# Kernel tuning notes

Hardware: AMD Instinct MI355X
Metric: run time of the kernel (lower is better)

The kernel has to match this reference:

```python
import jax, jax.numpy as jnp
import numpy as np

TEMPERATURE = 1.0
EXAGGERATION = 1.0


def setup_inputs() -> dict:
    key = jax.random.key(0)
    features = jax.random.normal(key, (8192, 128), dtype=jnp.float32)
    return {"features": features}


def _cauchy_sim(x, y):
    # 1 / ((cdist(x,y) * t)^2 + 1) == 1 / (t^2 * sq_dist + 1)
    sq = (
        jnp.sum(x * x, axis=1)[:, None]
        + jnp.sum(y * y, axis=1)[None, :]
        - 2.0 * (x @ y.T)
    )
    sq = jnp.maximum(sq, 0.0)  # numerical floor, matches cdist >= 0
    return 1.0 / (sq * (TEMPERATURE * TEMPERATURE) + 1.0)


def reference(features):
    batch_size = features.shape[0] // 2
    a = features[:batch_size]
    b = features[batch_size:]

    sim_aa = _cauchy_sim(a, a)  # [B, B]
    sim_bb = _cauchy_sim(b, b)  # [B, B]
    sim_ab = _cauchy_sim(a, b)  # [B, B]

    tempered_alignment = jnp.mean(jnp.log(jnp.diagonal(sim_ab)))

    self_mask = jnp.eye(batch_size, dtype=bool)
    sim_aa = jnp.where(self_mask, 0.0, sim_aa)
    sim_bb = jnp.where(self_mask, 0.0, sim_bb)

    # hstack((sim_ab.T, sim_bb)).sum(1) == sim_ab.sum(0) + sim_bb.sum(1)
    logsumexp_1 = jnp.mean(jnp.log(jnp.sum(sim_ab, axis=0) + jnp.sum(sim_bb, axis=1)))
    logsumexp_2 = jnp.mean(jnp.log(jnp.sum(sim_aa, axis=1) + jnp.sum(sim_ab, axis=1)))
    raw_uniformity = logsumexp_1 + logsumexp_2

    loss = -(EXAGGERATION * tempered_alignment - raw_uniformity / 2.0)
    return loss
```

## Files before the change

kernel.cpp:

```cpp
#include <hip/hip_runtime.h>
#include <hip/hip_bf16.h>
#include <hip/hip_fp8.h>

typedef float f32x4 __attribute__((ext_vector_type(4)));
typedef int   i32x4 __attribute__((ext_vector_type(4)));
typedef int   i32x8 __attribute__((ext_vector_type(8)));

static constexpr int D     = 128;
static constexpr int BATCH = 4096;
static constexpr int N     = 8192;
static constexpr int BT    = 128;
static constexpr int NT    = N / BT;
static constexpr int TRI   = NT * (NT + 1) / 2;
static constexpr int SCALE1 = 0x7F7F7F7F;

__device__ __forceinline__ void load_lds16(const void* g, void* l) {
    __builtin_amdgcn_global_load_lds(
        (const __attribute__((address_space(1))) unsigned int*)g,
        (__attribute__((address_space(3))) unsigned int*)l, 16, 0, 0);
}

__global__ __launch_bounds__(256) void prep_kernel(const float* __restrict__ f,
                                                   unsigned char* __restrict__ Fp8,
                                                   float* __restrict__ norms,
                                                   float* __restrict__ diag,
                                                   float* __restrict__ out) {
    if (blockIdx.x == 0 && threadIdx.x == 0) out[0] = 0.f;
    const int w = threadIdx.x >> 6, lane = threadIdx.x & 63;
    const int i = blockIdx.x * 4 + w;
    const float2 va = *(const float2*)(f + (size_t)i * D + lane * 2);
    const float2 vb = *(const float2*)(f + (size_t)(i + BATCH) * D + lane * 2);

    auto storeF = [&](int row, float x, float y) {
        union { unsigned char b[2]; unsigned short u; } pk;
        pk.b[0] = __hip_fp8_e4m3(x).__x;
        pk.b[1] = __hip_fp8_e4m3(y).__x;
        const size_t dst = (size_t)(row >> 7) * 16384 + (row & 127) * 128
                         + (((lane >> 3) ^ (row & 7)) << 4) + (lane & 7) * 2;
        *(unsigned short*)(Fp8 + dst) = pk.u;
    };
    storeF(i, va.x, va.y);
    storeF(i + BATCH, vb.x, vb.y);

    float na = va.x * va.x + va.y * va.y;
    float nb = vb.x * vb.x + vb.y * vb.y;
    const float dx = va.x - vb.x, dy = va.y - vb.y;
    float dd = dx * dx + dy * dy;
    #pragma unroll
    for (int m = 1; m <= 32; m <<= 1) {
        na += __shfl_xor(na, m); nb += __shfl_xor(nb, m); dd += __shfl_xor(dd, m);
    }
    if (lane == 0) {
        norms[i] = na; norms[i + BATCH] = nb;
        diag[i] = 1.f / (dd + 1.f);
    }
}

__global__ __launch_bounds__(256, 4) void tile_kernel(const unsigned char* __restrict__ Fp8,
                                                      const float* __restrict__ norms,
                                                      float* __restrict__ P) {
    const int bid = blockIdx.x;
    const int id = (bid & 7) * (TRI / 8) + (bid >> 3);
    int ti = (int)((sqrtf(8.f * (float)id + 1.f) - 1.f) * 0.5f);
    while ((ti + 1) * (ti + 2) / 2 <= id) ++ti;
    while (ti * (ti + 1) / 2 > id) --ti;
    const int tj = id - ti * (ti + 1) / 2;
    const bool diagblk = (ti == tj);

    __shared__ __align__(16) unsigned char As[16384];
    __shared__ __align__(16) unsigned char Bs[16384];
    __shared__ float colbuf[BT];

    const int tid = threadIdx.x, wv = tid >> 6, lane = tid & 63;
    const int lr = lane & 15, hk = lane >> 4;
    if (tid < BT) colbuf[tid] = 0.f;

    const unsigned char* Aimg = Fp8 + (size_t)ti * 16384;
    const unsigned char* Bimg = Fp8 + (size_t)tj * 16384;
    #pragma unroll
    for (int it = 0; it < 4; ++it)
        load_lds16(Aimg + (it * 256 + tid) * 16, As + it * 4096 + wv * 1024);
    #pragma unroll
    for (int it = 0; it < 4; ++it)
        load_lds16(Bimg + (it * 256 + tid) * 16, Bs + it * 4096 + wv * 1024);
    __syncthreads();

    auto frag = [&](const unsigned char* S, int rowbase) -> i32x8 {
        const int row = rowbase + lr;
        const i32x4 q0 = *(const i32x4*)(S + row * 128 + (((hk * 2 + 0) ^ (lr & 7)) << 4));
        const i32x4 q1 = *(const i32x4*)(S + row * 128 + (((hk * 2 + 1) ^ (lr & 7)) << 4));
        return __builtin_shufflevector(q0, q1, 0, 1, 2, 3, 4, 5, 6, 7);
    };

    f32x4 acc[2][8];
    #pragma unroll
    for (int i = 0; i < 2; ++i)
        #pragma unroll
        for (int j = 0; j < 8; ++j)
            acc[i][j] = (f32x4){0.f, 0.f, 0.f, 0.f};

    const i32x8 av0 = frag(As, wv * 32);
    const i32x8 av1 = frag(As, wv * 32 + 16);
    #pragma unroll
    for (int fj = 0; fj < 8; ++fj) {
        const i32x8 bv = frag(Bs, fj * 16);
        acc[0][fj] = __builtin_amdgcn_mfma_scale_f32_16x16x128_f8f6f4(
            av0, bv, acc[0][fj], 0, 0, 0, SCALE1, 0, SCALE1);
        acc[1][fj] = __builtin_amdgcn_mfma_scale_f32_16x16x128_f8f6f4(
            av1, bv, acc[1][fj], 0, 0, 0, SCALE1, 0, SCALE1);
    }

    float colN[8];
    #pragma unroll
    for (int fj = 0; fj < 8; ++fj)
        colN[fj] = norms[tj * BT + fj * 16 + lr];

    float* PR = P + ((size_t)ti * NT + tj) * BT;
    #pragma unroll
    for (int fi = 0; fi < 2; ++fi) {
        const int lrow = wv * 32 + fi * 16 + hk * 4;
        const f32x4 rN = *(const f32x4*)(norms + ti * BT + lrow);
        f32x4 rs = (f32x4){0.f, 0.f, 0.f, 0.f};
        #pragma unroll
        for (int fj = 0; fj < 8; ++fj) {
            const int lcol = fj * 16 + lr;
            #pragma unroll
            for (int r = 0; r < 4; ++r) {
                float sq = rN[r] + colN[fj] - 2.f * acc[fi][fj][r];
                sq = fmaxf(sq, 0.f);
                float sim = __builtin_amdgcn_rcpf(sq + 1.f);
                if (diagblk && (lrow + r == lcol)) sim = 0.f;
                rs[r] += sim;
                acc[fi][fj][r] = sim;
            }
        }
        #pragma unroll
        for (int r = 0; r < 4; ++r) {
            rs[r] += __shfl_xor(rs[r], 1);
            rs[r] += __shfl_xor(rs[r], 2);
            rs[r] += __shfl_xor(rs[r], 4);
            rs[r] += __shfl_xor(rs[r], 8);
        }
        if (lr == 0)
            *(f32x4*)(PR + lrow) = rs;
    }

    if (!diagblk) {
        #pragma unroll
        for (int fj = 0; fj < 8; ++fj) {
            float cs = 0.f;
            #pragma unroll
            for (int fi = 0; fi < 2; ++fi)
                #pragma unroll
                for (int r = 0; r < 4; ++r)
                    cs += acc[fi][fj][r];
            cs += __shfl_xor(cs, 16);
            cs += __shfl_xor(cs, 32);
            if (hk == 0)
                atomicAdd(&colbuf[fj * 16 + lr], cs);
        }
        __syncthreads();
        if (tid < BT)
            P[((size_t)tj * NT + ti) * BT + tid] = colbuf[tid];
    }
}

__global__ __launch_bounds__(128) void finalize_kernel(const float* __restrict__ P,
                                                       const float* __restrict__ diag,
                                                       float* __restrict__ out) {
    const int t = blockIdx.x;
    const int r = threadIdx.x;
    const float* base = P + (size_t)t * NT * BT + r;
    float s = 0.f;
    #pragma unroll 8
    for (int k = 0; k < NT; ++k) s += base[k * BT];
    const int i = t * BT + r;
    float term = 0.5f * __logf(s);
    if (i >= BATCH) term -= __logf(diag[i - BATCH]);
    #pragma unroll
    for (int m = 1; m <= 32; m <<= 1) term += __shfl_xor(term, m);
    if ((threadIdx.x & 63) == 0)
        atomicAdd(out, term / (float)BATCH);
}

extern "C" void kernel_launch(void* const* d_in, const int* in_sizes, int n_in,
                              void* d_out, int out_size, void* d_ws, size_t ws_size,
                              hipStream_t stream) {
    const float* feat = (const float*)d_in[0];
    char* ws = (char*)d_ws;
    unsigned char* Fp8 = (unsigned char*)ws;
    float* norms = (float*)(ws + (1u << 20));
    float* diag  = (float*)(ws + (1u << 20) + 32768);
    float* P     = (float*)(ws + (1u << 20) + 49152);
    float* out   = (float*)d_out;

    prep_kernel<<<BATCH / 4, 256, 0, stream>>>(feat, Fp8, norms, diag, out);
    tile_kernel<<<TRI, 256, 0, stream>>>(Fp8, norms, P);
    finalize_kernel<<<NT, 128, 0, stream>>>(P, diag, out);
}
```

Measured before the change: 78.72 us.

## Load A fragments directly from a fragment-packed global layout and split diagonal epilogue

Prep now writes a second FP8 copy of the features in an MFMA-fragment-packed order, so each wave loads its A operands straight into registers from global memory instead of staging the A tile through LDS. This halves LDS usage per block and removes the A LDS round trip. The epilogue is also split: off-diagonal blocks use a branch-free path that folds +1 into the row norms, clamps at 1 and fuses column sums, while diagonal blocks keep the masked path. The cost is extra workspace and prep-time writes, plus uncoalesced-ish direct global loads of A per wave.

```diff
diff --git a/kernel.cpp b/kernel.cpp
--- a/kernel.cpp
+++ b/kernel.cpp
@@ -3,6 +3,7 @@
 #include <hip/hip_fp8.h>
 
 typedef float f32x4 __attribute__((ext_vector_type(4)));
+typedef float f32x2 __attribute__((ext_vector_type(2)));
 typedef int   i32x4 __attribute__((ext_vector_type(4)));
 typedef int   i32x8 __attribute__((ext_vector_type(8)));
 
@@ -20,8 +21,16 @@
         (__attribute__((address_space(3))) unsigned int*)l, 16, 0, 0);
 }
 
+__device__ __forceinline__ f32x2 pkmax1(f32x2 a) {
+    return (f32x2){fmaxf(a[0], 1.f), fmaxf(a[1], 1.f)};
+}
+__device__ __forceinline__ f32x2 pkrcp(f32x2 a) {
+    return (f32x2){__builtin_amdgcn_rcpf(a[0]), __builtin_amdgcn_rcpf(a[1])};
+}
+
 __global__ __launch_bounds__(256) void prep_kernel(const float* __restrict__ f,
-                                                   unsigned char* __restrict__ Fp8,
+                                                   unsigned char* __restrict__ Apack,
+                                                   unsigned char* __restrict__ Bimg,
                                                    float* __restrict__ norms,
                                                    float* __restrict__ diag,
                                                    float* __restrict__ out) {
@@ -31,16 +40,20 @@
     const float2 va = *(const float2*)(f + (size_t)i * D + lane * 2);
     const float2 vb = *(const float2*)(f + (size_t)(i + BATCH) * D + lane * 2);
 
-    auto storeF = [&](int row, float x, float y) {
+    const int k = lane * 2;
+    auto storeBoth = [&](int row, float x, float y) {
         union { unsigned char b[2]; unsigned short u; } pk;
         pk.b[0] = __hip_fp8_e4m3(x).__x;
         pk.b[1] = __hip_fp8_e4m3(y).__x;
-        const size_t dst = (size_t)(row >> 7) * 16384 + (row & 127) * 128
-                         + (((lane >> 3) ^ (row & 7)) << 4) + (lane & 7) * 2;
-        *(unsigned short*)(Fp8 + dst) = pk.u;
+        const size_t bdst = (size_t)(row >> 7) * 16384 + (row & 127) * 128
+                          + (((k >> 4) ^ (row & 7)) << 4) + (k & 14);
+        *(unsigned short*)(Bimg + bdst) = pk.u;
+        const size_t adst = (size_t)(row >> 4) * 2048 + ((k >> 5) << 9)
+                          + ((row & 15) << 5) + (k & 31);
+        *(unsigned short*)(Apack + adst) = pk.u;
     };
-    storeF(i, va.x, va.y);
-    storeF(i + BATCH, vb.x, vb.y);
+    storeBoth(i, va.x, va.y);
+    storeBoth(i + BATCH, vb.x, vb.y);
 
     float na = va.x * va.x + va.y * va.y;
     float nb = vb.x * vb.x + vb.y * vb.y;
@@ -56,7 +69,8 @@
     }
 }
 
-__global__ __launch_bounds__(256, 4) void tile_kernel(const unsigned char* __restrict__ Fp8,
+__global__ __launch_bounds__(256, 4) void tile_kernel(const unsigned char* __restrict__ Apack,
+                                                      const unsigned char* __restrict__ Bimg,
                                                       const float* __restrict__ norms,
                                                       float* __restrict__ P) {
     const int bid = blockIdx.x;
@@ -67,28 +81,34 @@
     const int tj = id - ti * (ti + 1) / 2;
     const bool diagblk = (ti == tj);
 
-    __shared__ __align__(16) unsigned char As[16384];
     __shared__ __align__(16) unsigned char Bs[16384];
     __shared__ float colbuf[BT];
 
     const int tid = threadIdx.x, wv = tid >> 6, lane = tid & 63;
     const int lr = lane & 15, hk = lane >> 4;
+
+    const unsigned char* Ab = Apack + (size_t)(ti * 8 + wv * 2) * 2048;
+    const int ao = hk * 512 + lr * 32;
+    const i32x4 a00 = *(const i32x4*)(Ab + ao);
+    const i32x4 a01 = *(const i32x4*)(Ab + ao + 16);
+    const i32x4 a10 = *(const i32x4*)(Ab + 2048 + ao);
+    const i32x4 a11 = *(const i32x4*)(Ab + 2048 + ao + 16);
+
     if (tid < BT) colbuf[tid] = 0.f;
 
-    const unsigned char* Aimg = Fp8 + (size_t)ti * 16384;
-    const unsigned char* Bimg = Fp8 + (size_t)tj * 16384;
+    const unsigned char* Bimg_t = Bimg + (size_t)tj * 16384;
     #pragma unroll
     for (int it = 0; it < 4; ++it)
-        load_lds16(Aimg + (it * 256 + tid) * 16, As + it * 4096 + wv * 1024);
-    #pragma unroll
-    for (int it = 0; it < 4; ++it)
-        load_lds16(Bimg + (it * 256 + tid) * 16, Bs + it * 4096 + wv * 1024);
+        load_lds16(Bimg_t + (it * 256 + tid) * 16, Bs + it * 4096 + wv * 1024);
     __syncthreads();
 
-    auto frag = [&](const unsigned char* S, int rowbase) -> i32x8 {
+    const i32x8 av0 = __builtin_shufflevector(a00, a01, 0, 1, 2, 3, 4, 5, 6, 7);
+    const i32x8 av1 = __builtin_shufflevector(a10, a11, 0, 1, 2, 3, 4, 5, 6, 7);
+
+    auto frag = [&](int rowbase) -> i32x8 {
         const int row = rowbase + lr;
-        const i32x4 q0 = *(const i32x4*)(S + row * 128 + (((hk * 2 + 0) ^ (lr & 7)) << 4));
-        const i32x4 q1 = *(const i32x4*)(S + row * 128 + (((hk * 2 + 1) ^ (lr & 7)) << 4));
+        const i32x4 q0 = *(const i32x4*)(Bs + row * 128 + (((hk * 2 + 0) ^ (lr & 7)) << 4));
+        const i32x4 q1 = *(const i32x4*)(Bs + row * 128 + (((hk * 2 + 1) ^ (lr & 7)) << 4));
         return __builtin_shufflevector(q0, q1, 0, 1, 2, 3, 4, 5, 6, 7);
     };
 
@@ -99,69 +119,103 @@
         for (int j = 0; j < 8; ++j)
             acc[i][j] = (f32x4){0.f, 0.f, 0.f, 0.f};
 
-    const i32x8 av0 = frag(As, wv * 32);
-    const i32x8 av1 = frag(As, wv * 32 + 16);
     #pragma unroll
     for (int fj = 0; fj < 8; ++fj) {
-        const i32x8 bv = frag(Bs, fj * 16);
+        const i32x8 bv = frag(fj * 16);
         acc[0][fj] = __builtin_amdgcn_mfma_scale_f32_16x16x128_f8f6f4(
             av0, bv, acc[0][fj], 0, 0, 0, SCALE1, 0, SCALE1);
         acc[1][fj] = __builtin_amdgcn_mfma_scale_f32_16x16x128_f8f6f4(
             av1, bv, acc[1][fj], 0, 0, 0, SCALE1, 0, SCALE1);
     }
 
-    float colN[8];
-    #pragma unroll
-    for (int fj = 0; fj < 8; ++fj)
-        colN[fj] = norms[tj * BT + fj * 16 + lr];
-
     float* PR = P + ((size_t)ti * NT + tj) * BT;
-    #pragma unroll
-    for (int fi = 0; fi < 2; ++fi) {
-        const int lrow = wv * 32 + fi * 16 + hk * 4;
-        const f32x4 rN = *(const f32x4*)(norms + ti * BT + lrow);
-        f32x4 rs = (f32x4){0.f, 0.f, 0.f, 0.f};
+
+    if (!diagblk) {
+        float colN[8];
+        #pragma unroll
+        for (int fj = 0; fj < 8; ++fj)
+            colN[fj] = norms[tj * BT + fj * 16 + lr];
+
+        f32x2 rn[2][2], rs[2][2];
+        #pragma unroll
+        for (int fi = 0; fi < 2; ++fi) {
+            const int lrow = wv * 32 + fi * 16 + hk * 4;
+            const f32x4 rN = *(const f32x4*)(norms + ti * BT + lrow);
+            rn[fi][0] = (f32x2){rN[0] + 1.f, rN[1] + 1.f};
+            rn[fi][1] = (f32x2){rN[2] + 1.f, rN[3] + 1.f};
+            rs[fi][0] = (f32x2){0.f, 0.f};
+            rs[fi][1] = (f32x2){0.f, 0.f};
+        }
+
         #pragma unroll
         for (int fj = 0; fj < 8; ++fj) {
-            const int lcol = fj * 16 + lr;
+            const f32x2 cn2 = (f32x2){colN[fj], colN[fj]};
+            f32x2 cs = (f32x2){0.f, 0.f};
+            #pragma unroll
+            for (int fi = 0; fi < 2; ++fi) {
+                const f32x2 d01 = (f32x2){acc[fi][fj][0], acc[fi][fj][1]};
+                const f32x2 d23 = (f32x2){acc[fi][fj][2], acc[fi][fj][3]};
+                const f32x2 s01 = pkrcp(pkmax1(rn[fi][0] + cn2 - 2.f * d01));
+                const f32x2 s23 = pkrcp(pkmax1(rn[fi][1] + cn2 - 2.f * d23));
+                rs[fi][0] += s01; rs[fi][1] += s23;
+                cs += s01 + s23;
+            }
+            float csf = cs[0] + cs[1];
+            csf += __shfl_xor(csf, 16);
+            csf += __shfl_xor(csf, 32);
+            if (hk == 0)
+                atomicAdd(&colbuf[fj * 16 + lr], csf);
+        }
+
+        #pragma unroll
+        for (int fi = 0; fi < 2; ++fi) {
+            f32x4 rsv = (f32x4){rs[fi][0][0], rs[fi][0][1], rs[fi][1][0], rs[fi][1][1]};
             #pragma unroll
             for (int r = 0; r < 4; ++r) {
-                float sq = rN[r] + colN[fj] - 2.f * acc[fi][fj][r];
-                sq = fmaxf(sq, 0.f);
-                float sim = __builtin_amdgcn_rcpf(sq + 1.f);
-                if (diagblk && (lrow + r == lcol)) sim = 0.f;
-                rs[r] += sim;
-                acc[fi][fj][r] = sim;
-            }
-        }
-        #pragma unroll
-        for (int r = 0; r < 4; ++r) {
-            rs[r] += __shfl_xor(rs[r], 1);
-            rs[r] += __shfl_xor(rs[r], 2);
-            rs[r] += __shfl_xor(rs[r], 4);
-            rs[r] += __shfl_xor(rs[r], 8);
-        }
-        if (lr == 0)
-            *(f32x4*)(PR + lrow) = rs;
-    }
-
-    if (!diagblk) {
-        #pragma unroll
-        for (int fj = 0; fj < 8; ++fj) {
-            float cs = 0.f;
-            #pragma unroll
-            for (int fi = 0; fi < 2; ++fi)
-                #pragma unroll
-                for (int r = 0; r < 4; ++r)
-                    cs += acc[fi][fj][r];
-            cs += __shfl_xor(cs, 16);
-            cs += __shfl_xor(cs, 32);
-            if (hk == 0)
-                atomicAdd(&colbuf[fj * 16 + lr], cs);
-        }
+                rsv[r] += __shfl_xor(rsv[r], 1);
+                rsv[r] += __shfl_xor(rsv[r], 2);
+                rsv[r] += __shfl_xor(rsv[r], 4);
+                rsv[r] += __shfl_xor(rsv[r], 8);
+            }
+            if (lr == 0)
+                *(f32x4*)(PR + wv * 32 + fi * 16 + hk * 4) = rsv;
+        }
+
         __syncthreads();
         if (tid < BT)
             P[((size_t)tj * NT + ti) * BT + tid] = colbuf[tid];
+    } else {
+        float colN[8];
+        #pragma unroll
+        for (int fj = 0; fj < 8; ++fj)
+            colN[fj] = norms[tj * BT + fj * 16 + lr];
+        #pragma unroll
+        for (int fi = 0; fi < 2; ++fi) {
+            const int lrow = wv * 32 + fi * 16 + hk * 4;
+            const f32x4 rN = *(const f32x4*)(norms + ti * BT + lrow);
+            f32x4 rsv = (f32x4){0.f, 0.f, 0.f, 0.f};
+            #pragma unroll
+            for (int fj = 0; fj < 8; ++fj) {
+                const int lcol = fj * 16 + lr;
+                #pragma unroll
+                for (int r = 0; r < 4; ++r) {
+                    float sq = rN[r] + colN[fj] - 2.f * acc[fi][fj][r];
+                    sq = fmaxf(sq, 0.f);
+                    float sim = __builtin_amdgcn_rcpf(sq + 1.f);
+                    if (lrow + r == lcol) sim = 0.f;
+                    rsv[r] += sim;
+                }
+            }
+            #pragma unroll
+            for (int r = 0; r < 4; ++r) {
+                rsv[r] += __shfl_xor(rsv[r], 1);
+                rsv[r] += __shfl_xor(rsv[r], 2);
+                rsv[r] += __shfl_xor(rsv[r], 4);
+                rsv[r] += __shfl_xor(rsv[r], 8);
+            }
+            if (lr == 0)
+                *(f32x4*)(PR + lrow) = rsv;
+        }
     }
 }
 
@@ -188,13 +242,14 @@
                               hipStream_t stream) {
     const float* feat = (const float*)d_in[0];
     char* ws = (char*)d_ws;
-    unsigned char* Fp8 = (unsigned char*)ws;
-    float* norms = (float*)(ws + (1u << 20));
-    float* diag  = (float*)(ws + (1u << 20) + 32768);
-    float* P     = (float*)(ws + (1u << 20) + 49152);
+    unsigned char* Apack = (unsigned char*)ws;
+    unsigned char* Bimg  = (unsigned char*)(ws + (1u << 20));
+    float* norms = (float*)(ws + (2u << 20));
+    float* diag  = (float*)(ws + (2u << 20) + 32768);
+    float* P     = (float*)(ws + (2u << 20) + 49152);
     float* out   = (float*)d_out;
 
-    prep_kernel<<<BATCH / 4, 256, 0, stream>>>(feat, Fp8, norms, diag, out);
-    tile_kernel<<<TRI, 256, 0, stream>>>(Fp8, norms, P);
+    prep_kernel<<<BATCH / 4, 256, 0, stream>>>(feat, Apack, Bimg, norms, diag, out);
+    tile_kernel<<<TRI, 256, 0, stream>>>(Apack, Bimg, norms, P);
     finalize_kernel<<<NT, 128, 0, stream>>>(P, diag, out);
 }
```

Measured after the change: 82.70 us. 1.05x slower.
